# Optimization experiments

Measured on AMD Instinct MI355X. Metric: run time of the kernel, lower is better.

The kernel has to match this reference:

```python
import jax, jax.numpy as jnp
import numpy as np

# Constant from livnium.kernel.constants (assumed scalar; value taken as 1.0).
K_O = 1.0
EPS = 1e-12  # F.normalize default eps

B, D, C = 16384, 1024, 3
F_DIM = D + 10  # features = h_final (D) + 10 scalar features


def setup_inputs() -> dict:
    key = jax.random.key(0)
    ks = jax.random.split(key, 8)
    s1 = 1.0 / np.sqrt(F_DIM)
    return {
        "h_final": jax.random.normal(ks[0], (B, D), jnp.float32),
        "v_p": jax.random.normal(ks[1], (B, D), jnp.float32),
        "v_h": jax.random.normal(ks[2], (B, D), jnp.float32),
        "neutral_dir": jax.random.normal(ks[3], (D,), jnp.float32),
        "neutral_scale": jnp.array(1.0, jnp.float32),
        "w1": jax.random.normal(ks[4], (F_DIM, F_DIM), jnp.float32) * s1,
        "b1": jnp.zeros((F_DIM,), jnp.float32),
        "w2": jax.random.normal(ks[5], (C, F_DIM), jnp.float32) * s1,
        "b2": jnp.zeros((C,), jnp.float32),
    }


def _normalize(x, axis):
    n = jnp.linalg.norm(x, axis=axis, keepdims=True)
    return x / jnp.maximum(n, EPS)


def reference(h_final, v_p, v_h, neutral_dir, neutral_scale, w1, b1, w2, b2):
    v_p_n = _normalize(v_p, -1)                      # [B, D]
    v_h_n = _normalize(v_h, -1)                      # [B, D]
    nd_n = _normalize(neutral_dir, 0)                # [D]

    # alignment(): cosine of the unit vectors == batched dot product.
    align = jnp.sum(v_p_n * v_h_n, axis=-1, keepdims=True)        # [B, 1]
    opp = jnp.sum(-v_p_n * v_h_n, axis=-1, keepdims=True)          # [B, 1]
    align_neutral_p = neutral_scale * jnp.sum(v_p_n * nd_n, axis=-1, keepdims=True)
    align_neutral_h = neutral_scale * jnp.sum(v_h_n * nd_n, axis=-1, keepdims=True)

    energy = K_O * ((1.0 + align) * 0.5)
    expose_neg = (1.0 - align) * 0.5
    dist_p_h = jnp.linalg.norm(v_h - v_p, axis=-1, keepdims=True)
    r_p = jnp.linalg.norm(v_p, axis=-1, keepdims=True)
    r_h = jnp.linalg.norm(v_h, axis=-1, keepdims=True)
    r_final = jnp.linalg.norm(h_final, axis=-1, keepdims=True)

    features = jnp.concatenate(
        [h_final, align, opp, energy, expose_neg, dist_p_h,
         r_p, r_h, r_final, align_neutral_p, align_neutral_h], axis=-1)  # [B, D+10]

    hidden = jax.nn.relu(features @ w1.T + b1)
    logits = hidden @ w2.T + b2                      # [B, C]
    return logits
```

## Files before the change

kernel.cpp:

```cpp
#include <hip/hip_runtime.h>
#include <cstdint>
#include <cstddef>

#define B_ROWS 16384
#define D_DIM  1024
#define F_REAL 1034
#define N_PAD  1152
#define K_PAD  1088
#define NK     (K_PAD / 64)
#define EPSN   1e-12f

typedef __bf16 bf16x8 __attribute__((ext_vector_type(8)));
typedef float  f32x4  __attribute__((ext_vector_type(4)));
typedef unsigned short u16;

__device__ __forceinline__ u16 f2bf(float f) {
    __bf16 b = (__bf16)f;
    return __builtin_bit_cast(u16, b);
}

__global__ __launch_bounds__(256)
void prep_kernel(const float* __restrict__ h, const float* __restrict__ vp,
                 const float* __restrict__ vh, const float* __restrict__ nd,
                 const float* __restrict__ nsp, u16* __restrict__ A)
{
    const int row  = blockIdx.x * 4 + (threadIdx.x >> 6);
    const int lane = threadIdx.x & 63;
    const float4* hp  = (const float4*)(h  + (size_t)row * D_DIM);
    const float4* vpp = (const float4*)(vp + (size_t)row * D_DIM);
    const float4* vhp = (const float4*)(vh + (size_t)row * D_DIM);
    const float4* ndp = (const float4*)nd;
    u16* arow = A + (size_t)row * K_PAD;

    float4 pr[4], qr[4], fr[4], nr[4];
    #pragma unroll
    for (int c = 0; c < 4; ++c) pr[c] = vpp[lane + c * 64];
    #pragma unroll
    for (int c = 0; c < 4; ++c) qr[c] = vhp[lane + c * 64];
    #pragma unroll
    for (int c = 0; c < 4; ++c) fr[c] = hp[lane + c * 64];
    #pragma unroll
    for (int c = 0; c < 4; ++c) nr[c] = ndp[lane + c * 64];

    float s_pp = 0.f, s_hh = 0.f, s_pv = 0.f, s_ff = 0.f;
    float s_dd = 0.f, s_pn = 0.f, s_hn = 0.f, s_nn = 0.f;

    #pragma unroll
    for (int c = 0; c < 4; ++c) {
        float4 p = pr[c], q = qr[c], f = fr[c], n = nr[c];
        s_pp += p.x*p.x + p.y*p.y + p.z*p.z + p.w*p.w;
        s_hh += q.x*q.x + q.y*q.y + q.z*q.z + q.w*q.w;
        s_pv += p.x*q.x + p.y*q.y + p.z*q.z + p.w*q.w;
        s_ff += f.x*f.x + f.y*f.y + f.z*f.z + f.w*f.w;
        float dx = q.x-p.x, dy = q.y-p.y, dz = q.z-p.z, dw = q.w-p.w;
        s_dd += dx*dx + dy*dy + dz*dz + dw*dw;
        s_pn += p.x*n.x + p.y*n.y + p.z*n.z + p.w*n.w;
        s_hn += q.x*n.x + q.y*n.y + q.z*n.z + q.w*n.w;
        s_nn += n.x*n.x + n.y*n.y + n.z*n.z + n.w*n.w;

        ushort4 ho;
        ho.x = f2bf(f.x); ho.y = f2bf(f.y); ho.z = f2bf(f.z); ho.w = f2bf(f.w);
        *(ushort4*)(arow + (lane + c * 64) * 4) = ho;
    }

    #pragma unroll
    for (int m = 32; m >= 1; m >>= 1) {
        s_pp += __shfl_xor(s_pp, m, 64);
        s_hh += __shfl_xor(s_hh, m, 64);
        s_pv += __shfl_xor(s_pv, m, 64);
        s_ff += __shfl_xor(s_ff, m, 64);
        s_dd += __shfl_xor(s_dd, m, 64);
        s_pn += __shfl_xor(s_pn, m, 64);
        s_hn += __shfl_xor(s_hn, m, 64);
        s_nn += __shfl_xor(s_nn, m, 64);
    }

    if (lane == 0) {
        float np_ = sqrtf(s_pp), nh_ = sqrtf(s_hh), nf = sqrtf(s_ff);
        float npc = fmaxf(np_, EPSN), nhc = fmaxf(nh_, EPSN);
        float nnc = fmaxf(sqrtf(s_nn), EPSN);
        float align = s_pv / (npc * nhc);
        float ns = nsp[0];
        u16 fo[64];
        fo[0] = f2bf(align);
        fo[1] = f2bf(-align);
        fo[2] = f2bf(0.5f * (1.0f + align));
        fo[3] = f2bf(0.5f * (1.0f - align));
        fo[4] = f2bf(sqrtf(s_dd));
        fo[5] = f2bf(np_);
        fo[6] = f2bf(nh_);
        fo[7] = f2bf(nf);
        fo[8] = f2bf(ns * s_pn / (npc * nnc));
        fo[9] = f2bf(ns * s_hn / (nhc * nnc));
        #pragma unroll
        for (int i = 10; i < 64; ++i) fo[i] = 0;
        #pragma unroll
        for (int i = 0; i < 8; ++i)
            *(uint4*)(arow + D_DIM + i * 8) = *(uint4*)(fo + i * 8);
    }
}

__global__ __launch_bounds__(256)
void convw_kernel(const float* __restrict__ w1, u16* __restrict__ Bm)
{
    const int i = blockIdx.x;
    for (int j = threadIdx.x; j < K_PAD; j += 256) {
        float v = (i < F_REAL && j < F_REAL) ? w1[(size_t)i * F_REAL + j] : 0.0f;
        Bm[(size_t)i * K_PAD + j] = f2bf(v);
    }
}

__global__ __launch_bounds__(256)
void initout_kernel(const float* __restrict__ b2, float* __restrict__ out)
{
    int i = blockIdx.x * 256 + threadIdx.x;
    if (i < B_ROWS * 3) out[i] = b2[i % 3];
}

__global__ __launch_bounds__(256)
void gemm_kernel(const u16* __restrict__ A,
                 const u16* __restrict__ Bm,
                 const float* __restrict__ b1, const float* __restrict__ w2,
                 float* __restrict__ out)
{
    __shared__ __bf16 As[2 * 64 * 32];
    __shared__ __bf16 Bs[2 * 128 * 32];

    const int tid  = threadIdx.x;
    const int lane = tid & 63;
    const int wave = tid >> 6;
    const int wm = wave >> 1, wn = wave & 1;
    const int bm = blockIdx.x, bn = blockIdx.y;

    const u16* gaA;
    __bf16*    lA;
    {
        int row = tid >> 2;
        int kc  = (tid & 3) ^ (row & 3);
        gaA = A + (size_t)(bm * 64 + row) * K_PAD + kc * 8;
        lA  = As + tid * 8;
    }
    const u16* gaB[2];
    __bf16*    lB[2];
    #pragma unroll
    for (int o = 0; o < 2; ++o) {
        int s   = o * 256 + tid;
        int row = s >> 2;
        int kc  = (s & 3) ^ (row & 3);
        gaB[o] = Bm + (size_t)(bn * 128 + row) * K_PAD + kc * 8;
        lB[o]  = Bs + s * 8;
    }

    const int col  = lane & 15;
    const int quad = lane >> 4;
    const int swz  = quad ^ (col & 3);
    int aoff[2], boff[4];
    #pragma unroll
    for (int i = 0; i < 2; ++i)
        aoff[i] = ((wm * 32 + i * 16 + col) * 4 + swz) * 8;
    #pragma unroll
    for (int j = 0; j < 4; ++j)
        boff[j] = ((wn * 64 + j * 16 + col) * 4 + swz) * 8;

    f32x4 acc[2][4];
    #pragma unroll
    for (int i = 0; i < 2; ++i)
        #pragma unroll
        for (int j = 0; j < 4; ++j)
            acc[i][j] = (f32x4){0.f, 0.f, 0.f, 0.f};

    uint4 a0_0, a1_0, b00_0, b01_0, b10_0, b11_0;
    uint4 a0_1, a1_1, b00_1, b01_1, b10_1, b11_1;

#define LOAD_STAGE(st, ko)                                                    \
    do {                                                                      \
        a0_##st  = *(const uint4*)(gaA + (ko));                               \
        a1_##st  = *(const uint4*)(gaA + (ko) + 32);                          \
        b00_##st = *(const uint4*)(gaB[0] + (ko));                            \
        b01_##st = *(const uint4*)(gaB[0] + (ko) + 32);                       \
        b10_##st = *(const uint4*)(gaB[1] + (ko));                            \
        b11_##st = *(const uint4*)(gaB[1] + (ko) + 32);                       \
    } while (0)

#define WRITE_STAGE(st)                                                       \
    do {                                                                      \
        *(uint4*)(lA)           = a0_##st;                                    \
        *(uint4*)(lA + 2048)    = a1_##st;                                    \
        *(uint4*)(lB[0])        = b00_##st;                                   \
        *(uint4*)(lB[0] + 4096) = b01_##st;                                   \
        *(uint4*)(lB[1])        = b10_##st;                                   \
        *(uint4*)(lB[1] + 4096) = b11_##st;                                   \
    } while (0)

#define COMPUTE_TILE                                                          \
    do {                                                                      \
        _Pragma("unroll")                                                     \
        for (int h = 0; h < 2; ++h) {                                         \
            const __bf16* Ab = As + h * 2048;                                 \
            const __bf16* Bb = Bs + h * 4096;                                 \
            bf16x8 av[2], bv[4];                                              \
            _Pragma("unroll")                                                 \
            for (int i = 0; i < 2; ++i) av[i] = *(const bf16x8*)(Ab + aoff[i]); \
            _Pragma("unroll")                                                 \
            for (int j = 0; j < 4; ++j) bv[j] = *(const bf16x8*)(Bb + boff[j]); \
            _Pragma("unroll")                                                 \
            for (int i = 0; i < 2; ++i)                                       \
                _Pragma("unroll")                                             \
                for (int j = 0; j < 4; ++j)                                   \
                    acc[i][j] = __builtin_amdgcn_mfma_f32_16x16x32_bf16(      \
                                    av[i], bv[j], acc[i][j], 0, 0, 0);        \
        }                                                                     \
    } while (0)

    LOAD_STAGE(0, 0);
    LOAD_STAGE(1, 64);
    WRITE_STAGE(0);
    __syncthreads();

    for (int kt = 0; kt < NK; kt += 2) {
        if (kt + 2 < NK) LOAD_STAGE(0, (kt + 2) * 64);
        COMPUTE_TILE;
        if (kt + 1 < NK) {
            __syncthreads();
            WRITE_STAGE(1);
            __syncthreads();

            if (kt + 3 < NK) LOAD_STAGE(1, (kt + 3) * 64);
            COMPUTE_TILE;
            if (kt + 2 < NK) {
                __syncthreads();
                WRITE_STAGE(0);
                __syncthreads();
            }
        }
    }

    float bias[4], w20[4], w21[4], w22[4];
    #pragma unroll
    for (int ni = 0; ni < 4; ++ni) {
        int n = bn * 128 + wn * 64 + ni * 16 + col;
        bool v = n < F_REAL;
        bias[ni] = v ? b1[n] : 0.0f;
        w20[ni]  = v ? w2[n] : 0.0f;
        w21[ni]  = v ? w2[F_REAL + n] : 0.0f;
        w22[ni]  = v ? w2[2 * F_REAL + n] : 0.0f;
    }
    #pragma unroll
    for (int mi = 0; mi < 2; ++mi) {
        float c0[4] = {0,0,0,0}, c1[4] = {0,0,0,0}, c2[4] = {0,0,0,0};
        #pragma unroll
        for (int ni = 0; ni < 4; ++ni) {
            #pragma unroll
            for (int r = 0; r < 4; ++r) {
                float hd = fmaxf(acc[mi][ni][r] + bias[ni], 0.0f);
                c0[r] += hd * w20[ni];
                c1[r] += hd * w21[ni];
                c2[r] += hd * w22[ni];
            }
        }
        #pragma unroll
        for (int m = 8; m >= 1; m >>= 1) {
            #pragma unroll
            for (int r = 0; r < 4; ++r) {
                c0[r] += __shfl_xor(c0[r], m, 64);
                c1[r] += __shfl_xor(c1[r], m, 64);
                c2[r] += __shfl_xor(c2[r], m, 64);
            }
        }
        if (col == 0) {
            int gm = bm * 64 + wm * 32 + mi * 16 + quad * 4;
            #pragma unroll
            for (int r = 0; r < 4; ++r) {
                atomicAdd(out + (size_t)(gm + r) * 3 + 0, c0[r]);
                atomicAdd(out + (size_t)(gm + r) * 3 + 1, c1[r]);
                atomicAdd(out + (size_t)(gm + r) * 3 + 2, c2[r]);
            }
        }
    }
}

extern "C" void kernel_launch(void* const* d_in, const int* in_sizes, int n_in,
                              void* d_out, int out_size, void* d_ws, size_t ws_size,
                              hipStream_t stream)
{
    const float* h  = (const float*)d_in[0];
    const float* vp = (const float*)d_in[1];
    const float* vh = (const float*)d_in[2];
    const float* nd = (const float*)d_in[3];
    const float* ns = (const float*)d_in[4];
    const float* w1 = (const float*)d_in[5];
    const float* b1 = (const float*)d_in[6];
    const float* w2 = (const float*)d_in[7];
    const float* b2 = (const float*)d_in[8];
    float* out = (float*)d_out;

    u16* Afull = (u16*)d_ws;
    u16* Bfull = Afull + (size_t)B_ROWS * K_PAD;

    prep_kernel<<<B_ROWS / 4, 256, 0, stream>>>(h, vp, vh, nd, ns, Afull);
    convw_kernel<<<N_PAD, 256, 0, stream>>>(w1, Bfull);
    initout_kernel<<<(B_ROWS * 3 + 255) / 256, 256, 0, stream>>>(b2, out);
    gemm_kernel<<<dim3(B_ROWS / 64, N_PAD / 128), 256, 0, stream>>>(
        Afull, Bfull, b1, w2, out);
}
```

Measured before the change: 291.9 us.

## Enlarge GEMM tile to 128x128 with direct global-to-LDS loads; multi-row prep

The GEMM moves from a 64x128 to a 128x128 block tile, so each wave holds a 4x4 grid of accumulators, and it uses global_load_lds for double-buffered K=32 stages instead of staging through registers. The LDS swizzle pattern changes to match. The prep kernel now has each wave handle 4 rows, prefetching the next row's data in registers and computing the neutral-direction norm only once per wave. The aim is more data reuse per block, less register traffic and fewer launched blocks. The cost is higher register pressure and more barriers, since each K-step is now smaller.

Result: slower. 311.4 us (+6.7%).

```diff
diff --git a/kernel.cpp b/kernel.cpp
--- a/kernel.cpp
+++ b/kernel.cpp
@@ -7,7 +7,7 @@
 #define F_REAL 1034
 #define N_PAD  1152
 #define K_PAD  1088
-#define NK     (K_PAD / 64)
+#define NKT    34
 #define EPSN   1e-12f
 
 typedef __bf16 bf16x8 __attribute__((ext_vector_type(8)));
@@ -24,80 +24,105 @@
                  const float* __restrict__ vh, const float* __restrict__ nd,
                  const float* __restrict__ nsp, u16* __restrict__ A)
 {
-    const int row  = blockIdx.x * 4 + (threadIdx.x >> 6);
-    const int lane = threadIdx.x & 63;
-    const float4* hp  = (const float4*)(h  + (size_t)row * D_DIM);
-    const float4* vpp = (const float4*)(vp + (size_t)row * D_DIM);
-    const float4* vhp = (const float4*)(vh + (size_t)row * D_DIM);
+    const int tid  = threadIdx.x;
+    const int lane = tid & 63;
+    const int wg   = blockIdx.x * 4 + (tid >> 6);
+    const int r0   = wg * 4;
+
     const float4* ndp = (const float4*)nd;
-    u16* arow = A + (size_t)row * K_PAD;
-
-    float4 pr[4], qr[4], fr[4], nr[4];
-    #pragma unroll
-    for (int c = 0; c < 4; ++c) pr[c] = vpp[lane + c * 64];
-    #pragma unroll
-    for (int c = 0; c < 4; ++c) qr[c] = vhp[lane + c * 64];
-    #pragma unroll
-    for (int c = 0; c < 4; ++c) fr[c] = hp[lane + c * 64];
-    #pragma unroll
-    for (int c = 0; c < 4; ++c) nr[c] = ndp[lane + c * 64];
-
-    float s_pp = 0.f, s_hh = 0.f, s_pv = 0.f, s_ff = 0.f;
-    float s_dd = 0.f, s_pn = 0.f, s_hn = 0.f, s_nn = 0.f;
-
-    #pragma unroll
-    for (int c = 0; c < 4; ++c) {
-        float4 p = pr[c], q = qr[c], f = fr[c], n = nr[c];
-        s_pp += p.x*p.x + p.y*p.y + p.z*p.z + p.w*p.w;
-        s_hh += q.x*q.x + q.y*q.y + q.z*q.z + q.w*q.w;
-        s_pv += p.x*q.x + p.y*q.y + p.z*q.z + p.w*q.w;
-        s_ff += f.x*f.x + f.y*f.y + f.z*f.z + f.w*f.w;
-        float dx = q.x-p.x, dy = q.y-p.y, dz = q.z-p.z, dw = q.w-p.w;
-        s_dd += dx*dx + dy*dy + dz*dz + dw*dw;
-        s_pn += p.x*n.x + p.y*n.y + p.z*n.z + p.w*n.w;
-        s_hn += q.x*n.x + q.y*n.y + q.z*n.z + q.w*n.w;
-        s_nn += n.x*n.x + n.y*n.y + n.z*n.z + n.w*n.w;
-
-        ushort4 ho;
-        ho.x = f2bf(f.x); ho.y = f2bf(f.y); ho.z = f2bf(f.z); ho.w = f2bf(f.w);
-        *(ushort4*)(arow + (lane + c * 64) * 4) = ho;
-    }
-
-    #pragma unroll
-    for (int m = 32; m >= 1; m >>= 1) {
-        s_pp += __shfl_xor(s_pp, m, 64);
-        s_hh += __shfl_xor(s_hh, m, 64);
-        s_pv += __shfl_xor(s_pv, m, 64);
-        s_ff += __shfl_xor(s_ff, m, 64);
-        s_dd += __shfl_xor(s_dd, m, 64);
-        s_pn += __shfl_xor(s_pn, m, 64);
-        s_hn += __shfl_xor(s_hn, m, 64);
-        s_nn += __shfl_xor(s_nn, m, 64);
-    }
-
-    if (lane == 0) {
-        float np_ = sqrtf(s_pp), nh_ = sqrtf(s_hh), nf = sqrtf(s_ff);
-        float npc = fmaxf(np_, EPSN), nhc = fmaxf(nh_, EPSN);
-        float nnc = fmaxf(sqrtf(s_nn), EPSN);
-        float align = s_pv / (npc * nhc);
-        float ns = nsp[0];
-        u16 fo[64];
-        fo[0] = f2bf(align);
-        fo[1] = f2bf(-align);
-        fo[2] = f2bf(0.5f * (1.0f + align));
-        fo[3] = f2bf(0.5f * (1.0f - align));
-        fo[4] = f2bf(sqrtf(s_dd));
-        fo[5] = f2bf(np_);
-        fo[6] = f2bf(nh_);
-        fo[7] = f2bf(nf);
-        fo[8] = f2bf(ns * s_pn / (npc * nnc));
-        fo[9] = f2bf(ns * s_hn / (nhc * nnc));
-        #pragma unroll
-        for (int i = 10; i < 64; ++i) fo[i] = 0;
-        #pragma unroll
-        for (int i = 0; i < 8; ++i)
-            *(uint4*)(arow + D_DIM + i * 8) = *(uint4*)(fo + i * 8);
-    }
+    float4 n[4];
+    #pragma unroll
+    for (int c = 0; c < 4; ++c) n[c] = ndp[lane + c * 64];
+    const float ns = nsp[0];
+
+    float s_nn = 0.f;
+    #pragma unroll
+    for (int c = 0; c < 4; ++c)
+        s_nn += n[c].x*n[c].x + n[c].y*n[c].y + n[c].z*n[c].z + n[c].w*n[c].w;
+    #pragma unroll
+    for (int m = 32; m >= 1; m >>= 1) s_nn += __shfl_xor(s_nn, m, 64);
+    const float nnc = fmaxf(sqrtf(s_nn), EPSN);
+
+    float4 P[2][4], Q[2][4], F[2][4];
+
+#define LOADR(st, r)                                                          \
+    do {                                                                      \
+        const float4* vpp = (const float4*)(vp + (size_t)(r) * D_DIM);        \
+        const float4* vhp = (const float4*)(vh + (size_t)(r) * D_DIM);        \
+        const float4* hp  = (const float4*)(h  + (size_t)(r) * D_DIM);        \
+        _Pragma("unroll")                                                     \
+        for (int c = 0; c < 4; ++c) P[st][c] = vpp[lane + c * 64];            \
+        _Pragma("unroll")                                                     \
+        for (int c = 0; c < 4; ++c) Q[st][c] = vhp[lane + c * 64];            \
+        _Pragma("unroll")                                                     \
+        for (int c = 0; c < 4; ++c) F[st][c] = hp[lane + c * 64];             \
+    } while (0)
+
+    LOADR(0, r0);
+    #pragma unroll
+    for (int i = 0; i < 4; ++i) {
+        const int st = i & 1;
+        if (i + 1 < 4) LOADR(((i + 1) & 1), r0 + i + 1);
+        __builtin_amdgcn_sched_barrier(0);
+
+        float s_pp = 0.f, s_hh = 0.f, s_pv = 0.f, s_ff = 0.f;
+        float s_dd = 0.f, s_pn = 0.f, s_hn = 0.f;
+        #pragma unroll
+        for (int c = 0; c < 4; ++c) {
+            float4 p = P[st][c], q = Q[st][c], f = F[st][c], nn = n[c];
+            s_pp += p.x*p.x + p.y*p.y + p.z*p.z + p.w*p.w;
+            s_hh += q.x*q.x + q.y*q.y + q.z*q.z + q.w*q.w;
+            s_pv += p.x*q.x + p.y*q.y + p.z*q.z + p.w*q.w;
+            s_ff += f.x*f.x + f.y*f.y + f.z*f.z + f.w*f.w;
+            float dx = q.x-p.x, dy = q.y-p.y, dz = q.z-p.z, dw = q.w-p.w;
+            s_dd += dx*dx + dy*dy + dz*dz + dw*dw;
+            s_pn += p.x*nn.x + p.y*nn.y + p.z*nn.z + p.w*nn.w;
+            s_hn += q.x*nn.x + q.y*nn.y + q.z*nn.z + q.w*nn.w;
+        }
+
+        u16* arow = A + (size_t)(r0 + i) * K_PAD;
+        #pragma unroll
+        for (int c = 0; c < 4; ++c) {
+            ushort4 hc;
+            hc.x = f2bf(F[st][c].x); hc.y = f2bf(F[st][c].y);
+            hc.z = f2bf(F[st][c].z); hc.w = f2bf(F[st][c].w);
+            *(ushort4*)(arow + (lane + c * 64) * 4) = hc;
+        }
+
+        #pragma unroll
+        for (int m = 32; m >= 1; m >>= 1) {
+            s_pp += __shfl_xor(s_pp, m, 64);
+            s_hh += __shfl_xor(s_hh, m, 64);
+            s_pv += __shfl_xor(s_pv, m, 64);
+            s_ff += __shfl_xor(s_ff, m, 64);
+            s_dd += __shfl_xor(s_dd, m, 64);
+            s_pn += __shfl_xor(s_pn, m, 64);
+            s_hn += __shfl_xor(s_hn, m, 64);
+        }
+
+        if (lane == 0) {
+            float np_ = sqrtf(s_pp), nh_ = sqrtf(s_hh), nf = sqrtf(s_ff);
+            float npc = fmaxf(np_, EPSN), nhc = fmaxf(nh_, EPSN);
+            float align = s_pv / (npc * nhc);
+            u16 fo[64];
+            fo[0] = f2bf(align);
+            fo[1] = f2bf(-align);
+            fo[2] = f2bf(0.5f * (1.0f + align));
+            fo[3] = f2bf(0.5f * (1.0f - align));
+            fo[4] = f2bf(sqrtf(s_dd));
+            fo[5] = f2bf(np_);
+            fo[6] = f2bf(nh_);
+            fo[7] = f2bf(nf);
+            fo[8] = f2bf(ns * s_pn / (npc * nnc));
+            fo[9] = f2bf(ns * s_hn / (nhc * nnc));
+            #pragma unroll
+            for (int k = 10; k < 64; ++k) fo[k] = 0;
+            #pragma unroll
+            for (int k = 0; k < 8; ++k)
+                *(uint4*)(arow + D_DIM + k * 8) = *(uint4*)(fo + k * 8);
+        }
+    }
+#undef LOADR
 }
 
 __global__ __launch_bounds__(256)
@@ -123,7 +148,7 @@
                  const float* __restrict__ b1, const float* __restrict__ w2,
                  float* __restrict__ out)
 {
-    __shared__ __bf16 As[2 * 64 * 32];
+    __shared__ __bf16 As[2 * 128 * 32];
     __shared__ __bf16 Bs[2 * 128 * 32];
 
     const int tid  = threadIdx.x;
@@ -132,107 +157,78 @@
     const int wm = wave >> 1, wn = wave & 1;
     const int bm = blockIdx.x, bn = blockIdx.y;
 
-    const u16* gaA;
-    __bf16*    lA;
-    {
-        int row = tid >> 2;
-        int kc  = (tid & 3) ^ (row & 3);
-        gaA = A + (size_t)(bm * 64 + row) * K_PAD + kc * 8;
-        lA  = As + tid * 8;
-    }
-    const u16* gaB[2];
-    __bf16*    lB[2];
-    #pragma unroll
-    for (int o = 0; o < 2; ++o) {
-        int s   = o * 256 + tid;
+    const u16* srcA[2];
+    const u16* srcB[2];
+    #pragma unroll
+    for (int l = 0; l < 2; ++l) {
+        int s   = l * 256 + tid;
         int row = s >> 2;
-        int kc  = (s & 3) ^ (row & 3);
-        gaB[o] = Bm + (size_t)(bn * 128 + row) * K_PAD + kc * 8;
-        lB[o]  = Bs + s * 8;
-    }
+        int c   = (s & 3) ^ ((s >> 3) & 3);
+        srcA[l] = A  + (size_t)(bm * 128 + row) * K_PAD + c * 8;
+        srcB[l] = Bm + (size_t)(bn * 128 + row) * K_PAD + c * 8;
+    }
+    const int ldsbase = wave * 512;
+
+#define STAGE(buf, kt)                                                        \
+    do {                                                                      \
+        _Pragma("unroll")                                                     \
+        for (int l = 0; l < 2; ++l) {                                         \
+            __builtin_amdgcn_global_load_lds(                                 \
+                (const __attribute__((address_space(1))) void*)(srcA[l] + (kt) * 32), \
+                (__attribute__((address_space(3))) void*)(As + (buf) * 4096 + l * 2048 + ldsbase), \
+                16, 0, 0);                                                    \
+            __builtin_amdgcn_global_load_lds(                                 \
+                (const __attribute__((address_space(1))) void*)(srcB[l] + (kt) * 32), \
+                (__attribute__((address_space(3))) void*)(Bs + (buf) * 4096 + l * 2048 + ldsbase), \
+                16, 0, 0);                                                    \
+        }                                                                     \
+    } while (0)
 
     const int col  = lane & 15;
     const int quad = lane >> 4;
-    const int swz  = quad ^ (col & 3);
-    int aoff[2], boff[4];
-    #pragma unroll
-    for (int i = 0; i < 2; ++i)
-        aoff[i] = ((wm * 32 + i * 16 + col) * 4 + swz) * 8;
+    const int swz  = quad ^ ((col >> 1) & 3);
+    int aoff[4], boff[4];
+    #pragma unroll
+    for (int i = 0; i < 4; ++i)
+        aoff[i] = (wm * 64 + i * 16 + col) * 32 + swz * 8;
     #pragma unroll
     for (int j = 0; j < 4; ++j)
-        boff[j] = ((wn * 64 + j * 16 + col) * 4 + swz) * 8;
-
-    f32x4 acc[2][4];
-    #pragma unroll
-    for (int i = 0; i < 2; ++i)
+        boff[j] = (wn * 64 + j * 16 + col) * 32 + swz * 8;
+
+    f32x4 acc[4][4];
+    #pragma unroll
+    for (int i = 0; i < 4; ++i)
         #pragma unroll
         for (int j = 0; j < 4; ++j)
             acc[i][j] = (f32x4){0.f, 0.f, 0.f, 0.f};
 
-    uint4 a0_0, a1_0, b00_0, b01_0, b10_0, b11_0;
-    uint4 a0_1, a1_1, b00_1, b01_1, b10_1, b11_1;
-
-#define LOAD_STAGE(st, ko)                                                    \
+#define COMPUTE(buf)                                                          \
     do {                                                                      \
-        a0_##st  = *(const uint4*)(gaA + (ko));                               \
-        a1_##st  = *(const uint4*)(gaA + (ko) + 32);                          \
-        b00_##st = *(const uint4*)(gaB[0] + (ko));                            \
-        b01_##st = *(const uint4*)(gaB[0] + (ko) + 32);                       \
-        b10_##st = *(const uint4*)(gaB[1] + (ko));                            \
-        b11_##st = *(const uint4*)(gaB[1] + (ko) + 32);                       \
+        const __bf16* Ab = As + (buf) * 4096;                                 \
+        const __bf16* Bb = Bs + (buf) * 4096;                                 \
+        bf16x8 av[4], bv[4];                                                  \
+        _Pragma("unroll")                                                     \
+        for (int i = 0; i < 4; ++i) av[i] = *(const bf16x8*)(Ab + aoff[i]);   \
+        _Pragma("unroll")                                                     \
+        for (int j = 0; j < 4; ++j) bv[j] = *(const bf16x8*)(Bb + boff[j]);   \
+        _Pragma("unroll")                                                     \
+        for (int i = 0; i < 4; ++i)                                           \
+            _Pragma("unroll")                                                 \
+            for (int j = 0; j < 4; ++j)                                       \
+                acc[i][j] = __builtin_amdgcn_mfma_f32_16x16x32_bf16(          \
+                                av[i], bv[j], acc[i][j], 0, 0, 0);            \
     } while (0)
 
-#define WRITE_STAGE(st)                                                       \
-    do {                                                                      \
-        *(uint4*)(lA)           = a0_##st;                                    \
-        *(uint4*)(lA + 2048)    = a1_##st;                                    \
-        *(uint4*)(lB[0])        = b00_##st;                                   \
-        *(uint4*)(lB[0] + 4096) = b01_##st;                                   \
-        *(uint4*)(lB[1])        = b10_##st;                                   \
-        *(uint4*)(lB[1] + 4096) = b11_##st;                                   \
-    } while (0)
-
-#define COMPUTE_TILE                                                          \
-    do {                                                                      \
-        _Pragma("unroll")                                                     \
-        for (int h = 0; h < 2; ++h) {                                         \
-            const __bf16* Ab = As + h * 2048;                                 \
-            const __bf16* Bb = Bs + h * 4096;                                 \
-            bf16x8 av[2], bv[4];                                              \
-            _Pragma("unroll")                                                 \
-            for (int i = 0; i < 2; ++i) av[i] = *(const bf16x8*)(Ab + aoff[i]); \
-            _Pragma("unroll")                                                 \
-            for (int j = 0; j < 4; ++j) bv[j] = *(const bf16x8*)(Bb + boff[j]); \
-            _Pragma("unroll")                                                 \
-            for (int i = 0; i < 2; ++i)                                       \
-                _Pragma("unroll")                                             \
-                for (int j = 0; j < 4; ++j)                                   \
-                    acc[i][j] = __builtin_amdgcn_mfma_f32_16x16x32_bf16(      \
-                                    av[i], bv[j], acc[i][j], 0, 0, 0);        \
-        }                                                                     \
-    } while (0)
-
-    LOAD_STAGE(0, 0);
-    LOAD_STAGE(1, 64);
-    WRITE_STAGE(0);
+    STAGE(0, 0);
     __syncthreads();
 
-    for (int kt = 0; kt < NK; kt += 2) {
-        if (kt + 2 < NK) LOAD_STAGE(0, (kt + 2) * 64);
-        COMPUTE_TILE;
-        if (kt + 1 < NK) {
-            __syncthreads();
-            WRITE_STAGE(1);
-            __syncthreads();
-
-            if (kt + 3 < NK) LOAD_STAGE(1, (kt + 3) * 64);
-            COMPUTE_TILE;
-            if (kt + 2 < NK) {
-                __syncthreads();
-                WRITE_STAGE(0);
-                __syncthreads();
-            }
-        }
+    for (int kt = 0; kt < NKT; kt += 2) {
+        STAGE(1, kt + 1);
+        COMPUTE(0);
+        __syncthreads();
+        if (kt + 2 < NKT) STAGE(0, kt + 2);
+        COMPUTE(1);
+        __syncthreads();
     }
 
     float bias[4], w20[4], w21[4], w22[4];
@@ -246,7 +242,7 @@
         w22[ni]  = v ? w2[2 * F_REAL + n] : 0.0f;
     }
     #pragma unroll
-    for (int mi = 0; mi < 2; ++mi) {
+    for (int mi = 0; mi < 4; ++mi) {
         float c0[4] = {0,0,0,0}, c1[4] = {0,0,0,0}, c2[4] = {0,0,0,0};
         #pragma unroll
         for (int ni = 0; ni < 4; ++ni) {
@@ -268,7 +264,7 @@
             }
         }
         if (col == 0) {
-            int gm = bm * 64 + wm * 32 + mi * 16 + quad * 4;
+            int gm = bm * 128 + wm * 64 + mi * 16 + quad * 4;
             #pragma unroll
             for (int r = 0; r < 4; ++r) {
                 atomicAdd(out + (size_t)(gm + r) * 3 + 0, c0[r]);
@@ -277,6 +273,8 @@
             }
         }
     }
+#undef STAGE
+#undef COMPUTE
 }
 
 extern "C" void kernel_launch(void* const* d_in, const int* in_sizes, int n_in,
@@ -297,9 +295,9 @@
     u16* Afull = (u16*)d_ws;
     u16* Bfull = Afull + (size_t)B_ROWS * K_PAD;
 
-    prep_kernel<<<B_ROWS / 4, 256, 0, stream>>>(h, vp, vh, nd, ns, Afull);
+    prep_kernel<<<1024, 256, 0, stream>>>(h, vp, vh, nd, ns, Afull);
     convw_kernel<<<N_PAD, 256, 0, stream>>>(w1, Bfull);
     initout_kernel<<<(B_ROWS * 3 + 255) / 256, 256, 0, stream>>>(b2, out);
-    gemm_kernel<<<dim3(B_ROWS / 64, N_PAD / 128), 256, 0, stream>>>(
+    gemm_kernel<<<dim3(B_ROWS / 128, N_PAD / 128), 256, 0, stream>>>(
         Afull, Bfull, b1, w2, out);
 }
```
